# Performance work log

Hardware: AMD Instinct MI355X
Metric: run time of the kernel (lower is better)

The kernel has to match this reference:

```python
import jax, jax.numpy as jnp
import numpy as np
from jax import lax

EPS = 1e-5

# Straight-through identity binarization (torch code mutates .data, so autograd
# sees binarized values but grads flow as identity to the latent weights/inputs).
def ste_sign(x):
    return x + lax.stop_gradient(jnp.sign(x) - x)

# SignActivation: sign forward, hard-tanh-style gradient (zero where |i| > 1).
@jax.custom_vjp
def sign_act(x):
    return jnp.sign(x)

def _sa_fwd(x):
    return jnp.sign(x), x

def _sa_bwd(x, g):
    return (jnp.where(jnp.abs(x) <= 1.0, g, 0.0),)

sign_act.defvjp(_sa_fwd, _sa_bwd)

def bn2d(x, gamma, beta):
    # training-mode BatchNorm2d: batch stats over (N,H,W), biased variance
    mean = jnp.mean(x, axis=(0, 2, 3), keepdims=True)
    var = jnp.var(x, axis=(0, 2, 3), keepdims=True)
    xn = (x - mean) * lax.rsqrt(var + EPS)
    return xn * gamma.reshape(1, -1, 1, 1) + beta.reshape(1, -1, 1, 1)

def bn1d(x, gamma, beta):
    mean = jnp.mean(x, axis=0, keepdims=True)
    var = jnp.var(x, axis=0, keepdims=True)
    xn = (x - mean) * lax.rsqrt(var + EPS)
    return xn * gamma[None, :] + beta[None, :]

def conv2d(x, w, stride, pad):
    return lax.conv_general_dilated(
        x, w, window_strides=(stride, stride),
        padding=((pad, pad), (pad, pad)),
        dimension_numbers=("NCHW", "OIHW", "NCHW"))


def setup_inputs() -> dict:
    key = jax.random.key(0)
    ks = jax.random.split(key, 4)
    width = 0.01
    x = jax.random.normal(ks[0], (8192, 1, 28, 28), dtype=jnp.float32)
    w1 = jax.random.normal(ks[1], (32, 1, 5, 5), dtype=jnp.float32) * width
    w2 = jax.random.normal(ks[2], (64, 32, 4, 4), dtype=jnp.float32) * width
    w3 = jax.random.normal(ks[3], (10, 64 * 64), dtype=jnp.float32) * width
    g1 = jnp.ones((32,), jnp.float32); b1 = jnp.zeros((32,), jnp.float32)
    g2 = jnp.ones((64,), jnp.float32); b2 = jnp.zeros((64,), jnp.float32)
    g3 = jnp.ones((10,), jnp.float32); b3 = jnp.zeros((10,), jnp.float32)
    return {"x": x, "w1": w1, "g1": g1, "b1": b1,
            "w2": w2, "g2": g2, "b2": b2,
            "w3": w3, "g3": g3, "b3": b3}


def reference(x, w1, g1, b1, w2, g2, b2, w3, g3, b3):
    # cv1: input channels = 1 != 3 -> input binarized; weight binarized
    h = conv2d(ste_sign(x), ste_sign(w1), stride=2, pad=2)   # [B,32,14,14]
    h = bn2d(h, g1, b1)
    h = sign_act(h)
    # cv2: input channels 32 != 3 -> binarized (no-op on +-1 values)
    h = conv2d(ste_sign(h), ste_sign(w2), stride=2, pad=2)   # [B,64,8,8]
    h = bn2d(h, g2, b2)
    h = sign_act(h)
    h = h.reshape(h.shape[0], -1)                            # [B,4096]
    # fc3: features 4096 != 784 -> binarized (no-op on +-1 values)
    h = jnp.dot(ste_sign(h), ste_sign(w3).T)                 # [B,10]
    h = bn1d(h, g3, b3)
    return h
```

## Files before the change

kernel.cpp:

```cpp
#include <hip/hip_runtime.h>
#include <stdint.h>


#define NB 8192
typedef unsigned long long ull;

#define OFF_C1  ((size_t)0)
#define SZ_C1   ((size_t)NB*6272)
#define OFF_C2  (OFF_C1 + SZ_C1)
#define SZ_C2   ((size_t)NB*4096)
#define OFF_FC  (OFF_C2 + SZ_C2)
#define SZ_FC   ((size_t)NB*10*4)
#define OFF_S1  (OFF_FC + SZ_FC)
#define OFF_S2  (OFF_S1 + 2048)
#define OFF_S3  (OFF_S2 + 8192)
#define OFF_W2B (OFF_S3 + 2048)
#define OFF_W3B (OFF_W2B + 4096)

__device__ inline void mk_thresh(double s, double t, int &T, int &flip) {
    if (s > 0.0) {
        int v = (int)floor(-t / s) - 2;
        for (int c = 0; c < 6; ++c) { if (s * (double)v + t > 0.0) break; ++v; }
        T = v; flip = 0;
    } else if (s < 0.0) {
        int v = (int)floor(-t / s) - 2;
        for (int c = 0; c < 6; ++c) { if (!(s * (double)v + t > 0.0)) break; ++v; }
        T = v; flip = 1;
    } else { T = -200; flip = (t > 0.0) ? 0 : 1; }
}
__device__ inline int clampT(int T, int lim) {
    return (T < -lim) ? -lim : (T > lim) ? lim : T;
}

__global__ __launch_bounds__(256) void kP_pack(
    const float* __restrict__ w2, const float* __restrict__ w3,
    ull* __restrict__ w2bT, ull* __restrict__ w3b)
{
    const int t = blockIdx.x*256 + threadIdx.x;
    if (t < 512) {
        const int idx = t >> 6, k = t & 63;
        const int u = idx >> 1, pr = idx & 1;
        uint32_t lo = 0u, hi = 0u;
        #pragma unroll 8
        for (int c = 0; c < 32; ++c) {
            const float* wp = w2 + (((k*32 + c)*4 + u)*4 + 2*pr);
            lo |= (wp[0] > 0.f ? 1u : 0u) << c;
            hi |= (wp[1] > 0.f ? 1u : 0u) << c;
        }
        w2bT[t] = (ull)lo | ((ull)hi << 32);
    } else if (t < 1152) {
        const int w = t - 512;
        const float* wp = w3 + (size_t)(w >> 6)*4096 + (size_t)(w & 63)*64;
        ull bits = 0ull;
        #pragma unroll 16
        for (int k = 0; k < 64; ++k)
            bits |= (ull)(wp[k] > 0.f ? 1 : 0) << k;
        w3b[w] = bits;
    }
}

__global__ __launch_bounds__(256) void kA_conv1(
    const float* __restrict__ x, const float* __restrict__ w1,
    int8_t* __restrict__ c1out, int* __restrict__ stats1)
{
    const int tid = threadIdx.x, lane = tid & 63, wv = tid >> 6;

    __shared__ ull sxb[4][16];
    __shared__ uint32_t wfilt[32];
    __shared__ uint32_t outb[4][1568];
    __shared__ int lsum[32], lsq[32];

    if (tid < 32) {
        uint32_t f = 0u;
        #pragma unroll
        for (int q = 0; q < 25; ++q) f |= (w1[tid*25 + q] > 0.f ? 1u : 0u) << q;
        wfilt[tid] = f;
        lsum[tid] = 0; lsq[tid] = 0;
    }
    __syncthreads();
    const int n = blockIdx.x*4 + wv;
    #pragma unroll
    for (int t = 0; t < 13; ++t) {
        const int idx = t*64 + lane;
        const float v = (idx < 784) ? x[(size_t)n*784 + idx] : -1.f;
        const ull bal = __ballot(v > 0.f);
        if (lane == t) sxb[wv][t] = bal;
    }
    if (lane == 13) sxb[wv][13] = 0ull;
    for (int t = 0; t < 4; ++t) {
        const int p = t*64 + lane;
        if (p < 196) {
            const int i = p / 14, j = p - i*14;
            const uint32_t cmask = (j == 0) ? 0x1Cu : (j == 13) ? 0x0Fu : 0x1Fu;
            uint32_t win = 0u, vm = 0u;
            #pragma unroll
            for (int u = 0; u < 5; ++u) {
                const int r = 2*i + u - 2;
                if (r >= 0 && r < 28) {
                    const int bp = 28*r, w0 = bp >> 6, sh = bp & 63;
                    const ull a = sxb[wv][w0], b = sxb[wv][w0+1];
                    uint32_t row = (uint32_t)((a >> sh) | ((b << 1) << (63 - sh)));
                    row = (row & 0x0FFFFFFFu) << 2;
                    win |= ((row >> (2*j)) & 31u) << (5*u);
                    vm  |= cmask << (5*u);
                }
            }
            const int nv = __popc(vm);
            uint32_t dw[8];
            #pragma unroll
            for (int d = 0; d < 8; ++d) dw[d] = 0u;
            #pragma unroll
            for (int c = 0; c < 32; ++c) {
                const int diff = __popc((win ^ wfilt[c]) & vm);
                const int o = nv - 2*diff;
                dw[c >> 2] |= (uint32_t)(o & 255) << (8*(c & 3));
            }
            #pragma unroll
            for (int d = 0; d < 8; ++d) outb[wv][p*8 + d] = dw[d];
        }
    }
    {
        int4* dst = (int4*)(c1out + (size_t)n*6272);
        const int4* src = (const int4*)&outb[wv][0];
        #pragma unroll
        for (int t = 0; t < 7; ++t) {
            const int idx = t*64 + lane;
            if (idx < 392) dst[idx] = src[idx];
        }
    }
    {
        int s4[4] = {0,0,0,0}, q4[4] = {0,0,0,0};
        const uint32_t* ob32 = &outb[wv][0];
        #pragma unroll
        for (int t = 0; t < 25; ++t) {
            const int idx = t*64 + lane;
            if (idx < 1568) {
                const uint32_t dwv = ob32[idx];
                #pragma unroll
                for (int qq = 0; qq < 4; ++qq) {
                    const int v = (int)((int8_t)(dwv >> (8*qq)));
                    s4[qq] += v; q4[qq] += v*v;
                }
            }
        }
        #pragma unroll
        for (int off = 8; off <= 32; off <<= 1) {
            #pragma unroll
            for (int qq = 0; qq < 4; ++qq) {
                s4[qq] += __shfl_xor(s4[qq], off);
                q4[qq] += __shfl_xor(q4[qq], off);
            }
        }
        if (lane < 8) {
            #pragma unroll
            for (int qq = 0; qq < 4; ++qq) {
                atomicAdd(&lsum[lane*4 + qq], s4[qq]);
                atomicAdd(&lsq[lane*4 + qq], q4[qq]);
            }
        }
    }
    __syncthreads();
    if (tid < 32) {
        const int shard = blockIdx.x & 7;
        atomicAdd(&stats1[(shard*32 + tid)*2 + 0], lsum[tid]);
        atomicAdd(&stats1[(shard*32 + tid)*2 + 1], lsq[tid]);
    }
}

__global__ __launch_bounds__(256) void kB_conv2(
    const int8_t* __restrict__ c1out, const int* __restrict__ stats1,
    const float* __restrict__ gm1, const float* __restrict__ bt1,
    const ull* __restrict__ w2bT,
    int8_t* __restrict__ c2out, ull* __restrict__ stats2)
{
    __shared__ ull BwU[4][14][8];
    __shared__ int sT1[4][32];
    __shared__ uint32_t cw[4][64][17];
    __shared__ int ssum[64], ssq[64];
    const int tid = threadIdx.x, lane = tid & 63, wv = tid >> 6;
    const int n = blockIdx.x*4 + wv;

    ull W[8];
    #pragma unroll
    for (int idx = 0; idx < 8; ++idx) W[idx] = w2bT[idx*64 + lane];

    if (tid < 64) { ssum[tid] = 0; ssq[tid] = 0; }
    int fl = 0;
    if (lane < 32) {
        long long s = 0, q = 0;
        for (int sh = 0; sh < 8; ++sh) {
            s += stats1[(sh*32 + lane)*2 + 0];
            q += stats1[(sh*32 + lane)*2 + 1];
        }
        const double N = 8192.0 * 196.0;
        const double mean = (double)s / N;
        const double var  = (double)q / N - mean*mean;
        const double a = (double)gm1[lane] / sqrt(var + 1e-5);
        const double b = (double)bt1[lane] - mean*a;
        int T; mk_thresh(a, b, T, fl);
        sT1[wv][lane] = clampT(T, 26);
    }
    const uint32_t flipn1 = ~(uint32_t)__ballot(fl != 0);
    __syncthreads();

    for (int t = lane; t < 196; t += 64) {
        const int r = t / 14, c = t - r*14;
        const uint4* src = (const uint4*)(c1out + ((size_t)n*196 + t)*32);
        const uint4 lo4 = src[0], hi4 = src[1];
        const uint32_t wsrc[8] = {lo4.x, lo4.y, lo4.z, lo4.w, hi4.x, hi4.y, hi4.z, hi4.w};
        uint32_t neg = 0u;
        #pragma unroll
        for (int d = 0; d < 8; ++d) {
            #pragma unroll
            for (int qq = 0; qq < 4; ++qq) {
                const int ch = d*4 + qq;
                const int v = (int)((int8_t)(wsrc[d] >> (8*qq)));
                neg |= ((uint32_t)(v - sT1[wv][ch]) >> 31) << ch;
            }
        }
        ((uint32_t*)&BwU[wv][r][0])[c] = neg ^ flipn1;
    }
    int s = 0, q = 0;
    #pragma unroll
    for (int i = 0; i < 8; ++i) {
        uint32_t packA = 0u;
        #pragma unroll
        for (int j = 0; j < 8; ++j) {
            int D = 0, nw = 0;
            #pragma unroll
            for (int u = 0; u < 4; ++u) {
                const int r = 2*i + u - 2;
                if (r < 0 || r > 13) continue;
                const ull* row = &BwU[wv][r][0];
                if (j >= 1) { D += __popcll(row[j-1] ^ W[2*u+0]); ++nw; }
                if (j <= 6) { D += __popcll(row[j]   ^ W[2*u+1]); ++nw; }
            }
            const int o = 32*nw - D;
            s += o; q += o*o;
            packA |= (uint32_t)(o & 255) << (8*(j & 3));
            if ((j & 3) == 3) { cw[wv][lane][2*i + (j >> 2)] = packA; packA = 0u; }
        }
    }
    atomicAdd(&ssum[lane], s);
    atomicAdd(&ssq[lane], q);
    {
        uint32_t* dst = (uint32_t*)(c2out + (size_t)n*4096);
        #pragma unroll
        for (int t = 0; t < 16; ++t) {
            const int g = t*64 + lane;
            dst[g] = cw[wv][g >> 4][g & 15];
        }
    }
    __syncthreads();
    if (tid < 64) {
        const int shard = blockIdx.x & 7;
        atomicAdd(&stats2[(shard*64 + tid)*2 + 0], (ull)(long long)ssum[tid]);
        atomicAdd(&stats2[(shard*64 + tid)*2 + 1], (ull)(long long)ssq[tid]);
    }
}

__global__ __launch_bounds__(256) void kC_fc(
    const int8_t* __restrict__ c2o, const float* __restrict__ gm2,
    const float* __restrict__ bt2, const ull* __restrict__ stats2,
    const ull* __restrict__ w3b,
    int* __restrict__ fc, ull* __restrict__ stats3)
{
    __shared__ int fco[4][10];
    __shared__ int s3[10], q3[10];
    const int tid = threadIdx.x, lane = tid & 63, wv = tid >> 6;
    if (tid < 10) { s3[tid] = 0; q3[tid] = 0; }
    int T2, fl;
    {
        long long ss = 0, qq = 0;
        for (int sh = 0; sh < 8; ++sh) {
            ss += (long long)stats2[(sh*64 + lane)*2 + 0];
            qq += (long long)stats2[(sh*64 + lane)*2 + 1];
        }
        const double N = 8192.0 * 64.0;
        const double mh = (double)ss / N;
        const double vh = (double)qq / N - mh*mh;
        const double a = (double)gm2[lane] / sqrt(4.0*vh + 1e-5);
        const double b = (double)bt2[lane] - 2.0*mh*a;
        int T; mk_thresh(2.0*a, b, T, fl);
        T2 = clampT(T, 200);
    }
    const ull flipn2 = ~__ballot(fl != 0);
    const int n = blockIdx.x*4 + wv;
    const uint4* src = (const uint4*)(c2o + (size_t)n*4096 + lane*64);
    uint32_t neglo = 0u, neghi = 0u;
    #pragma unroll
    for (int r4 = 0; r4 < 4; ++r4) {
        const uint4 v4 = src[r4];
        const uint32_t wsrc[4] = {v4.x, v4.y, v4.z, v4.w};
        #pragma unroll
        for (int cc = 0; cc < 4; ++cc) {
            #pragma unroll
            for (int b = 0; b < 4; ++b) {
                const int p = r4*16 + cc*4 + b;
                const int v = (int)((int8_t)(wsrc[cc] >> (8*b)));
                const uint32_t bit = (uint32_t)(v - T2) >> 31;
                if (p < 32) neglo |= bit << p; else neghi |= bit << (p - 32);
            }
        }
    }
    const ull myw = ((ull)neglo | ((ull)neghi << 32)) ^ flipn2;
    uint32_t pk[5];
    #pragma unroll
    for (int t = 0; t < 5; ++t) {
        const uint32_t pa = (uint32_t)__popcll(myw ^ w3b[(2*t+0)*64 + lane]);
        const uint32_t pb = (uint32_t)__popcll(myw ^ w3b[(2*t+1)*64 + lane]);
        pk[t] = pa | (pb << 16);
    }
    #pragma unroll
    for (int off = 32; off >= 1; off >>= 1) {
        #pragma unroll
        for (int t = 0; t < 5; ++t) pk[t] += __shfl_xor(pk[t], off);
    }
    if (lane == 0) {
        #pragma unroll
        for (int m = 0; m < 10; ++m) {
            const int tot = (pk[m >> 1] >> (16*(m & 1))) & 0xFFFF;
            fco[wv][m] = 4096 - 2*tot;
        }
    }
    __syncthreads();
    if (tid < 40) {
        const int li = tid / 10, m = tid - li*10;
        const int o = fco[li][m];
        fc[(size_t)(blockIdx.x*4 + li)*10 + m] = o;
        atomicAdd(&s3[m], o);
        atomicAdd(&q3[m], o*o);
    }
    __syncthreads();
    if (tid < 10) {
        const int shard = blockIdx.x & 7;
        atomicAdd(&stats3[(shard*10 + tid)*2 + 0], (ull)(long long)s3[tid]);
        atomicAdd(&stats3[(shard*10 + tid)*2 + 1], (ull)(long long)q3[tid]);
    }
}

__global__ __launch_bounds__(256) void kD_apply(
    const int* __restrict__ fc, const float* __restrict__ gm3,
    const float* __restrict__ bt3, const ull* __restrict__ stats3,
    float* __restrict__ out)
{
    __shared__ float a3[10], b3[10];
    const int tid = threadIdx.x;
    if (tid < 10) {
        long long s = 0, q = 0;
        for (int sh = 0; sh < 8; ++sh) {
            s += (long long)stats3[(sh*10 + tid)*2 + 0];
            q += (long long)stats3[(sh*10 + tid)*2 + 1];
        }
        const double N = 8192.0;
        const double mean = (double)s / N;
        const double var  = (double)q / N - mean*mean;
        const double a = (double)gm3[tid] / sqrt(var + 1e-5);
        a3[tid] = (float)a;
        b3[tid] = (float)((double)bt3[tid] - mean*a);
    }
    __syncthreads();
    const int e = blockIdx.x*256 + tid;
    if (e < NB*10) {
        const int m = e % 10;
        out[e] = fmaf(a3[m], (float)fc[e], b3[m]);
    }
}

extern "C" void kernel_launch(void* const* d_in, const int* in_sizes, int n_in,
                              void* d_out, int out_size, void* d_ws, size_t ws_size,
                              hipStream_t stream)
{
    const float* x   = (const float*)d_in[0];
    const float* w1  = (const float*)d_in[1];
    const float* gm1 = (const float*)d_in[2];
    const float* bt1 = (const float*)d_in[3];
    const float* w2  = (const float*)d_in[4];
    const float* gm2 = (const float*)d_in[5];
    const float* bt2 = (const float*)d_in[6];
    const float* w3  = (const float*)d_in[7];
    const float* gm3 = (const float*)d_in[8];
    const float* bt3 = (const float*)d_in[9];
    char* ws = (char*)d_ws;
    int8_t* c1o = (int8_t*)(ws + OFF_C1);
    int8_t* c2o = (int8_t*)(ws + OFF_C2);
    int*    fcb = (int*)(ws + OFF_FC);
    int*    s1  = (int*)(ws + OFF_S1);
    ull*    s2  = (ull*)(ws + OFF_S2);
    ull*    s3  = (ull*)(ws + OFF_S3);
    ull*    w2bp = (ull*)(ws + OFF_W2B);
    ull*    w3bp = (ull*)(ws + OFF_W3B);

    (void)hipMemsetAsync(ws + OFF_S1, 0, 12288, stream);
    kP_pack <<<5,    256, 0, stream>>>(w2, w3, w2bp, w3bp);
    kA_conv1<<<2048, 256, 0, stream>>>(x, w1, c1o, s1);
    kB_conv2<<<2048, 256, 0, stream>>>(c1o, s1, gm1, bt1, w2bp, c2o, s2);
    kC_fc   <<<2048, 256, 0, stream>>>(c2o, gm2, bt2, s2, w3bp, fcb, s3);
    kD_apply<<<320,  256, 0, stream>>>(fcb, gm3, bt3, s3, (float*)d_out);
}
```

Before: 182.6 us.

## Fold weight packing into conv1 launch and register-stage conv2 rows

Merges the weight-packing kernel into the conv1 launch as five extra blocks that return early, which saves one kernel launch and its gap. In conv2, the binarized input rows are now stored as 32-bit words and pairs of rows are preloaded into registers with 128-bit LDS reads. The popcounts then run on 32-bit halves against split weight registers, which cuts repeated shared-memory loads in the inner loop. The cost is higher register pressure in conv2 (two 32-word buffers), which could lower occupancy.

Measured after the change: 181.4 us. About the same (-0.6%).

```diff
diff --git a/kernel.cpp b/kernel.cpp
--- a/kernel.cpp
+++ b/kernel.cpp
@@ -32,38 +32,38 @@
     return (T < -lim) ? -lim : (T > lim) ? lim : T;
 }
 
-__global__ __launch_bounds__(256) void kP_pack(
+__global__ __launch_bounds__(256) void kA_conv1(
+    const float* __restrict__ x, const float* __restrict__ w1,
     const float* __restrict__ w2, const float* __restrict__ w3,
+    int8_t* __restrict__ c1out, int* __restrict__ stats1,
     ull* __restrict__ w2bT, ull* __restrict__ w3b)
 {
-    const int t = blockIdx.x*256 + threadIdx.x;
-    if (t < 512) {
-        const int idx = t >> 6, k = t & 63;
-        const int u = idx >> 1, pr = idx & 1;
-        uint32_t lo = 0u, hi = 0u;
-        #pragma unroll 8
-        for (int c = 0; c < 32; ++c) {
-            const float* wp = w2 + (((k*32 + c)*4 + u)*4 + 2*pr);
-            lo |= (wp[0] > 0.f ? 1u : 0u) << c;
-            hi |= (wp[1] > 0.f ? 1u : 0u) << c;
-        }
-        w2bT[t] = (ull)lo | ((ull)hi << 32);
-    } else if (t < 1152) {
-        const int w = t - 512;
-        const float* wp = w3 + (size_t)(w >> 6)*4096 + (size_t)(w & 63)*64;
-        ull bits = 0ull;
-        #pragma unroll 16
-        for (int k = 0; k < 64; ++k)
-            bits |= (ull)(wp[k] > 0.f ? 1 : 0) << k;
-        w3b[w] = bits;
-    }
-}
-
-__global__ __launch_bounds__(256) void kA_conv1(
-    const float* __restrict__ x, const float* __restrict__ w1,
-    int8_t* __restrict__ c1out, int* __restrict__ stats1)
-{
     const int tid = threadIdx.x, lane = tid & 63, wv = tid >> 6;
+
+    if (blockIdx.x >= 2048) {
+        const int t = (blockIdx.x - 2048)*256 + tid;
+        if (t < 512) {
+            const int idx = t >> 6, k = t & 63;
+            const int u = idx >> 1, pr = idx & 1;
+            uint32_t lo = 0u, hi = 0u;
+            #pragma unroll 8
+            for (int c = 0; c < 32; ++c) {
+                const float* wp = w2 + (((k*32 + c)*4 + u)*4 + 2*pr);
+                lo |= (wp[0] > 0.f ? 1u : 0u) << c;
+                hi |= (wp[1] > 0.f ? 1u : 0u) << c;
+            }
+            w2bT[t] = (ull)lo | ((ull)hi << 32);
+        } else if (t < 1152) {
+            const int w = t - 512;
+            const float* wp = w3 + (size_t)(w >> 6)*4096 + (size_t)(w & 63)*64;
+            ull bits = 0ull;
+            #pragma unroll 16
+            for (int k = 0; k < 64; ++k)
+                bits |= (ull)(wp[k] > 0.f ? 1 : 0) << k;
+            w3b[w] = bits;
+        }
+        return;
+    }
 
     __shared__ ull sxb[4][16];
     __shared__ uint32_t wfilt[32];
@@ -173,16 +173,19 @@
     const ull* __restrict__ w2bT,
     int8_t* __restrict__ c2out, ull* __restrict__ stats2)
 {
-    __shared__ ull BwU[4][14][8];
+    __shared__ uint32_t BwU[4][14][16];
     __shared__ int sT1[4][32];
     __shared__ uint32_t cw[4][64][17];
     __shared__ int ssum[64], ssq[64];
     const int tid = threadIdx.x, lane = tid & 63, wv = tid >> 6;
     const int n = blockIdx.x*4 + wv;
 
-    ull W[8];
-    #pragma unroll
-    for (int idx = 0; idx < 8; ++idx) W[idx] = w2bT[idx*64 + lane];
+    uint32_t Wlo[8], Whi[8];
+    #pragma unroll
+    for (int idx = 0; idx < 8; ++idx) {
+        const uint2 w = ((const uint2*)w2bT)[idx*64 + lane];
+        Wlo[idx] = w.x; Whi[idx] = w.y;
+    }
 
     if (tid < 64) { ssum[tid] = 0; ssq[tid] = 0; }
     int fl = 0;
@@ -218,29 +221,60 @@
                 neg |= ((uint32_t)(v - sT1[wv][ch]) >> 31) << ch;
             }
         }
-        ((uint32_t*)&BwU[wv][r][0])[c] = neg ^ flipn1;
+        BwU[wv][r][c] = neg ^ flipn1;
+    }
+
+    uint32_t PA[32], PB[32];
+#define LOADP(BUF, K)                                                          \
+    {                                                                          \
+        const uint4* r0 = (const uint4*)&BwU[wv][2*(K)][0];                    \
+        const uint4* r1 = (const uint4*)&BwU[wv][2*(K)+1][0];                  \
+        _Pragma("unroll")                                                      \
+        for (int tt = 0; tt < 4; ++tt) {                                       \
+            const uint4 v0 = r0[tt];                                           \
+            BUF[4*tt+0] = v0.x; BUF[4*tt+1] = v0.y;                            \
+            BUF[4*tt+2] = v0.z; BUF[4*tt+3] = v0.w;                            \
+            const uint4 v1 = r1[tt];                                           \
+            BUF[16+4*tt+0] = v1.x; BUF[16+4*tt+1] = v1.y;                      \
+            BUF[16+4*tt+2] = v1.z; BUF[16+4*tt+3] = v1.w;                      \
+        }                                                                      \
+    }
+#define UT(BUF, RO, UU)                                                        \
+    {                                                                          \
+        if (j >= 1) { D += __popc(BUF[(RO)*16 + 2*j-2] ^ Wlo[2*(UU)])          \
+                         + __popc(BUF[(RO)*16 + 2*j-1] ^ Whi[2*(UU)]);   ++nw; } \
+        if (j <= 6) { D += __popc(BUF[(RO)*16 + 2*j]   ^ Wlo[2*(UU)+1])        \
+                         + __popc(BUF[(RO)*16 + 2*j+1] ^ Whi[2*(UU)+1]); ++nw; } \
     }
     int s = 0, q = 0;
+    LOADP(PA, 0)
     #pragma unroll
     for (int i = 0; i < 8; ++i) {
-        uint32_t packA = 0u;
+        if (i >= 1 && i <= 6) {
+            if (i & 1) { LOADP(PB, i) } else { LOADP(PA, i) }
+        }
+        uint32_t o0 = 0u, o1 = 0u;
         #pragma unroll
         for (int j = 0; j < 8; ++j) {
             int D = 0, nw = 0;
-            #pragma unroll
-            for (int u = 0; u < 4; ++u) {
-                const int r = 2*i + u - 2;
-                if (r < 0 || r > 13) continue;
-                const ull* row = &BwU[wv][r][0];
-                if (j >= 1) { D += __popcll(row[j-1] ^ W[2*u+0]); ++nw; }
-                if (j <= 6) { D += __popcll(row[j]   ^ W[2*u+1]); ++nw; }
+            if (i >= 1) {
+                if ((i-1) & 1) { UT(PB, 0, 0) UT(PB, 1, 1) }
+                else           { UT(PA, 0, 0) UT(PA, 1, 1) }
+            }
+            if (i <= 6) {
+                if (i & 1) { UT(PB, 0, 2) UT(PB, 1, 3) }
+                else       { UT(PA, 0, 2) UT(PA, 1, 3) }
             }
             const int o = 32*nw - D;
             s += o; q += o*o;
-            packA |= (uint32_t)(o & 255) << (8*(j & 3));
-            if ((j & 3) == 3) { cw[wv][lane][2*i + (j >> 2)] = packA; packA = 0u; }
-        }
-    }
+            if (j < 4) o0 |= (uint32_t)(o & 255) << (8*j);
+            else       o1 |= (uint32_t)(o & 255) << (8*(j-4));
+        }
+        cw[wv][lane][2*i]     = o0;
+        cw[wv][lane][2*i + 1] = o1;
+    }
+#undef LOADP
+#undef UT
     atomicAdd(&ssum[lane], s);
     atomicAdd(&ssq[lane], q);
     {
@@ -392,8 +426,7 @@
     ull*    w3bp = (ull*)(ws + OFF_W3B);
 
     (void)hipMemsetAsync(ws + OFF_S1, 0, 12288, stream);
-    kP_pack <<<5,    256, 0, stream>>>(w2, w3, w2bp, w3bp);
-    kA_conv1<<<2048, 256, 0, stream>>>(x, w1, c1o, s1);
+    kA_conv1<<<2053, 256, 0, stream>>>(x, w1, w2, w3, c1o, s1, w2bp, w3bp);
     kB_conv2<<<2048, 256, 0, stream>>>(c1o, s1, gm1, bt1, w2bp, c2o, s2);
     kC_fc   <<<2048, 256, 0, stream>>>(c2o, gm2, bt2, s2, w3bp, fcb, s3);
     kD_apply<<<320,  256, 0, stream>>>(fcb, gm3, bt3, s3, (float*)d_out);
```

## Fold weight packing into conv1, write conv1 output directly, batch 4 samples per FC wave

Applied to the files above, without the earlier changes.

The weight-packing kernel becomes five extra blocks of the conv1 launch, which removes one kernel launch. Conv1 now stores its int8 outputs straight to global memory instead of staging them in shared memory and copying. Per-channel statistics are reduced from a transposed shared layout into per-wave partial sums, which replaces the shared-memory atomics. The FC kernel handles four samples per wave and reuses each packed weight load across them, with a quarter as many blocks, which amortises the threshold setup and the weight loads but lowers parallelism.

Result: slower. 191.0 us (+4.6%).

```diff
diff --git a/kernel.cpp b/kernel.cpp
--- a/kernel.cpp
+++ b/kernel.cpp
@@ -32,50 +32,49 @@
     return (T < -lim) ? -lim : (T > lim) ? lim : T;
 }
 
-__global__ __launch_bounds__(256) void kP_pack(
+__global__ __launch_bounds__(256) void kA_conv1(
+    const float* __restrict__ x, const float* __restrict__ w1,
     const float* __restrict__ w2, const float* __restrict__ w3,
+    int8_t* __restrict__ c1out, int* __restrict__ stats1,
     ull* __restrict__ w2bT, ull* __restrict__ w3b)
 {
-    const int t = blockIdx.x*256 + threadIdx.x;
-    if (t < 512) {
-        const int idx = t >> 6, k = t & 63;
-        const int u = idx >> 1, pr = idx & 1;
-        uint32_t lo = 0u, hi = 0u;
-        #pragma unroll 8
-        for (int c = 0; c < 32; ++c) {
-            const float* wp = w2 + (((k*32 + c)*4 + u)*4 + 2*pr);
-            lo |= (wp[0] > 0.f ? 1u : 0u) << c;
-            hi |= (wp[1] > 0.f ? 1u : 0u) << c;
-        }
-        w2bT[t] = (ull)lo | ((ull)hi << 32);
-    } else if (t < 1152) {
-        const int w = t - 512;
-        const float* wp = w3 + (size_t)(w >> 6)*4096 + (size_t)(w & 63)*64;
-        ull bits = 0ull;
-        #pragma unroll 16
-        for (int k = 0; k < 64; ++k)
-            bits |= (ull)(wp[k] > 0.f ? 1 : 0) << k;
-        w3b[w] = bits;
-    }
-}
-
-__global__ __launch_bounds__(256) void kA_conv1(
-    const float* __restrict__ x, const float* __restrict__ w1,
-    int8_t* __restrict__ c1out, int* __restrict__ stats1)
-{
     const int tid = threadIdx.x, lane = tid & 63, wv = tid >> 6;
+
+    if (blockIdx.x >= 2048) {
+        const int t = (blockIdx.x - 2048)*256 + tid;
+        if (t < 512) {
+            const int idx = t >> 6, k = t & 63;
+            const int u = idx >> 1, pr = idx & 1;
+            uint32_t lo = 0u, hi = 0u;
+            #pragma unroll 8
+            for (int c = 0; c < 32; ++c) {
+                const float* wp = w2 + (((k*32 + c)*4 + u)*4 + 2*pr);
+                lo |= (wp[0] > 0.f ? 1u : 0u) << c;
+                hi |= (wp[1] > 0.f ? 1u : 0u) << c;
+            }
+            w2bT[t] = (ull)lo | ((ull)hi << 32);
+        } else if (t < 1152) {
+            const int w = t - 512;
+            const float* wp = w3 + (size_t)(w >> 6)*4096 + (size_t)(w & 63)*64;
+            ull bits = 0ull;
+            #pragma unroll 16
+            for (int k = 0; k < 64; ++k)
+                bits |= (ull)(wp[k] > 0.f ? 1 : 0) << k;
+            w3b[w] = bits;
+        }
+        return;
+    }
 
     __shared__ ull sxb[4][16];
     __shared__ uint32_t wfilt[32];
-    __shared__ uint32_t outb[4][1568];
-    __shared__ int lsum[32], lsq[32];
+    __shared__ uint32_t obT[4][8][196];
+    __shared__ int lpart[4][8][4][2];
 
     if (tid < 32) {
         uint32_t f = 0u;
         #pragma unroll
         for (int q = 0; q < 25; ++q) f |= (w1[tid*25 + q] > 0.f ? 1u : 0u) << q;
         wfilt[tid] = f;
-        lsum[tid] = 0; lsq[tid] = 0;
     }
     __syncthreads();
     const int n = blockIdx.x*4 + wv;
@@ -115,55 +114,56 @@
                 const int o = nv - 2*diff;
                 dw[c >> 2] |= (uint32_t)(o & 255) << (8*(c & 3));
             }
-            #pragma unroll
-            for (int d = 0; d < 8; ++d) outb[wv][p*8 + d] = dw[d];
-        }
-    }
-    {
-        int4* dst = (int4*)(c1out + (size_t)n*6272);
-        const int4* src = (const int4*)&outb[wv][0];
-        #pragma unroll
-        for (int t = 0; t < 7; ++t) {
-            const int idx = t*64 + lane;
-            if (idx < 392) dst[idx] = src[idx];
-        }
-    }
-    {
+            uint4* dst = (uint4*)(c1out + (size_t)n*6272 + (size_t)p*32);
+            dst[0] = make_uint4(dw[0], dw[1], dw[2], dw[3]);
+            dst[1] = make_uint4(dw[4], dw[5], dw[6], dw[7]);
+            #pragma unroll
+            for (int d = 0; d < 8; ++d) obT[wv][d][p] = dw[d];
+        }
+    }
+    #pragma unroll
+    for (int d = 0; d < 8; ++d) {
         int s4[4] = {0,0,0,0}, q4[4] = {0,0,0,0};
-        const uint32_t* ob32 = &outb[wv][0];
-        #pragma unroll
-        for (int t = 0; t < 25; ++t) {
-            const int idx = t*64 + lane;
-            if (idx < 1568) {
-                const uint32_t dwv = ob32[idx];
+        #pragma unroll
+        for (int t = 0; t < 4; ++t) {
+            const int pp = t*64 + lane;
+            if (pp < 196) {
+                const uint32_t v32 = obT[wv][d][pp];
                 #pragma unroll
                 for (int qq = 0; qq < 4; ++qq) {
-                    const int v = (int)((int8_t)(dwv >> (8*qq)));
+                    const int v = (int)((int8_t)(v32 >> (8*qq)));
                     s4[qq] += v; q4[qq] += v*v;
                 }
             }
         }
         #pragma unroll
-        for (int off = 8; off <= 32; off <<= 1) {
+        for (int off = 1; off <= 32; off <<= 1) {
             #pragma unroll
             for (int qq = 0; qq < 4; ++qq) {
                 s4[qq] += __shfl_xor(s4[qq], off);
                 q4[qq] += __shfl_xor(q4[qq], off);
             }
         }
-        if (lane < 8) {
+        if (lane == 0) {
             #pragma unroll
             for (int qq = 0; qq < 4; ++qq) {
-                atomicAdd(&lsum[lane*4 + qq], s4[qq]);
-                atomicAdd(&lsq[lane*4 + qq], q4[qq]);
+                lpart[wv][d][qq][0] = s4[qq];
+                lpart[wv][d][qq][1] = q4[qq];
             }
         }
     }
     __syncthreads();
     if (tid < 32) {
+        const int d = tid >> 2, qq = tid & 3;
+        int s = 0, q = 0;
+        #pragma unroll
+        for (int w = 0; w < 4; ++w) {
+            s += lpart[w][d][qq][0];
+            q += lpart[w][d][qq][1];
+        }
         const int shard = blockIdx.x & 7;
-        atomicAdd(&stats1[(shard*32 + tid)*2 + 0], lsum[tid]);
-        atomicAdd(&stats1[(shard*32 + tid)*2 + 1], lsq[tid]);
+        atomicAdd(&stats1[(shard*32 + tid)*2 + 0], s);
+        atomicAdd(&stats1[(shard*32 + tid)*2 + 1], q);
     }
 }
 
@@ -265,7 +265,7 @@
     const ull* __restrict__ w3b,
     int* __restrict__ fc, ull* __restrict__ stats3)
 {
-    __shared__ int fco[4][10];
+    __shared__ int fco[16][10];
     __shared__ int s3[10], q3[10];
     const int tid = threadIdx.x, lane = tid & 63, wv = tid >> 6;
     if (tid < 10) { s3[tid] = 0; q3[tid] = 0; }
@@ -285,49 +285,62 @@
         T2 = clampT(T, 200);
     }
     const ull flipn2 = ~__ballot(fl != 0);
-    const int n = blockIdx.x*4 + wv;
-    const uint4* src = (const uint4*)(c2o + (size_t)n*4096 + lane*64);
-    uint32_t neglo = 0u, neghi = 0u;
-    #pragma unroll
-    for (int r4 = 0; r4 < 4; ++r4) {
-        const uint4 v4 = src[r4];
-        const uint32_t wsrc[4] = {v4.x, v4.y, v4.z, v4.w};
-        #pragma unroll
-        for (int cc = 0; cc < 4; ++cc) {
-            #pragma unroll
-            for (int b = 0; b < 4; ++b) {
-                const int p = r4*16 + cc*4 + b;
-                const int v = (int)((int8_t)(wsrc[cc] >> (8*b)));
-                const uint32_t bit = (uint32_t)(v - T2) >> 31;
-                if (p < 32) neglo |= bit << p; else neghi |= bit << (p - 32);
-            }
-        }
-    }
-    const ull myw = ((ull)neglo | ((ull)neghi << 32)) ^ flipn2;
-    uint32_t pk[5];
+    const int n0 = blockIdx.x*16 + wv*4;
+    ull myw[4];
+    #pragma unroll
+    for (int im = 0; im < 4; ++im) {
+        const uint4* src = (const uint4*)(c2o + (size_t)(n0+im)*4096 + lane*64);
+        uint32_t neglo = 0u, neghi = 0u;
+        #pragma unroll
+        for (int r4 = 0; r4 < 4; ++r4) {
+            const uint4 v4 = src[r4];
+            const uint32_t wsrc[4] = {v4.x, v4.y, v4.z, v4.w};
+            #pragma unroll
+            for (int cc = 0; cc < 4; ++cc) {
+                #pragma unroll
+                for (int b = 0; b < 4; ++b) {
+                    const int p = r4*16 + cc*4 + b;
+                    const int v = (int)((int8_t)(wsrc[cc] >> (8*b)));
+                    const uint32_t bit = (uint32_t)(v - T2) >> 31;
+                    if (p < 32) neglo |= bit << p; else neghi |= bit << (p - 32);
+                }
+            }
+        }
+        myw[im] = ((ull)neglo | ((ull)neghi << 32)) ^ flipn2;
+    }
+    uint32_t pk[4][5];
     #pragma unroll
     for (int t = 0; t < 5; ++t) {
-        const uint32_t pa = (uint32_t)__popcll(myw ^ w3b[(2*t+0)*64 + lane]);
-        const uint32_t pb = (uint32_t)__popcll(myw ^ w3b[(2*t+1)*64 + lane]);
-        pk[t] = pa | (pb << 16);
+        const ull wA = w3b[(2*t+0)*64 + lane];
+        const ull wB = w3b[(2*t+1)*64 + lane];
+        #pragma unroll
+        for (int im = 0; im < 4; ++im) {
+            const uint32_t pa = (uint32_t)__popcll(myw[im] ^ wA);
+            const uint32_t pb = (uint32_t)__popcll(myw[im] ^ wB);
+            pk[im][t] = pa | (pb << 16);
+        }
     }
     #pragma unroll
     for (int off = 32; off >= 1; off >>= 1) {
         #pragma unroll
-        for (int t = 0; t < 5; ++t) pk[t] += __shfl_xor(pk[t], off);
+        for (int im = 0; im < 4; ++im)
+            #pragma unroll
+            for (int t = 0; t < 5; ++t) pk[im][t] += __shfl_xor(pk[im][t], off);
     }
     if (lane == 0) {
         #pragma unroll
-        for (int m = 0; m < 10; ++m) {
-            const int tot = (pk[m >> 1] >> (16*(m & 1))) & 0xFFFF;
-            fco[wv][m] = 4096 - 2*tot;
-        }
-    }
-    __syncthreads();
-    if (tid < 40) {
+        for (int im = 0; im < 4; ++im)
+            #pragma unroll
+            for (int m = 0; m < 10; ++m) {
+                const int tot = (pk[im][m >> 1] >> (16*(m & 1))) & 0xFFFF;
+                fco[wv*4 + im][m] = 4096 - 2*tot;
+            }
+    }
+    __syncthreads();
+    if (tid < 160) {
         const int li = tid / 10, m = tid - li*10;
         const int o = fco[li][m];
-        fc[(size_t)(blockIdx.x*4 + li)*10 + m] = o;
+        fc[(size_t)(blockIdx.x*16 + li)*10 + m] = o;
         atomicAdd(&s3[m], o);
         atomicAdd(&q3[m], o*o);
     }
@@ -392,9 +405,8 @@
     ull*    w3bp = (ull*)(ws + OFF_W3B);
 
     (void)hipMemsetAsync(ws + OFF_S1, 0, 12288, stream);
-    kP_pack <<<5,    256, 0, stream>>>(w2, w3, w2bp, w3bp);
-    kA_conv1<<<2048, 256, 0, stream>>>(x, w1, c1o, s1);
+    kA_conv1<<<2053, 256, 0, stream>>>(x, w1, w2, w3, c1o, s1, w2bp, w3bp);
     kB_conv2<<<2048, 256, 0, stream>>>(c1o, s1, gm1, bt1, w2bp, c2o, s2);
-    kC_fc   <<<2048, 256, 0, stream>>>(c2o, gm2, bt2, s2, w3bp, fcb, s3);
+    kC_fc   <<<512,  256, 0, stream>>>(c2o, gm2, bt2, s2, w3bp, fcb, s3);
     kD_apply<<<320,  256, 0, stream>>>(fcb, gm3, bt3, s3, (float*)d_out);
 }
```
